# Kernel optimization log

Hardware: AMD Instinct MI355X
Metric: run time of the kernel (lower is better)

## Reference

```python
import jax, jax.numpy as jnp
import numpy as np

LN_EPS = 1e-5


def _layer_norm(x, scale, bias):
    mu = jnp.mean(x, axis=-1, keepdims=True)
    var = jnp.mean(jnp.square(x - mu), axis=-1, keepdims=True)
    return (x - mu) * jax.lax.rsqrt(var + LN_EPS) * scale + bias


def setup_inputs() -> dict:
    key = jax.random.key(0)
    B, N, C_Z, C_H = 1, 512, 128, 128
    ks = jax.random.split(key, 8)
    s = 1.0 / np.sqrt(C_Z)
    inp = {
        "z": jax.random.normal(ks[0], (B, N, N, C_Z), dtype=jnp.float32),
        "mask": jnp.ones((B, N, N), dtype=jnp.float32),
        # gated / plain projections from c_z -> c_hidden
        "w_a_p": jax.random.normal(ks[1], (C_Z, C_H), dtype=jnp.float32) * s,
        "b_a_p": jnp.zeros((C_H,), dtype=jnp.float32),
        "w_a_g": jnp.zeros((C_Z, C_H), dtype=jnp.float32),  # gating init: zeros, bias ones
        "b_a_g": jnp.ones((C_H,), dtype=jnp.float32),
        "w_b_p": jax.random.normal(ks[2], (C_Z, C_H), dtype=jnp.float32) * s,
        "b_b_p": jnp.zeros((C_H,), dtype=jnp.float32),
        "w_b_g": jnp.zeros((C_Z, C_H), dtype=jnp.float32),
        "b_b_g": jnp.ones((C_H,), dtype=jnp.float32),
        # output gate c_z -> c_z (gating init)
        "w_g": jnp.zeros((C_Z, C_Z), dtype=jnp.float32),
        "b_g": jnp.ones((C_Z,), dtype=jnp.float32),
        # final projection c_hidden -> c_z ('final' init: zeros; use small randn for a nontrivial test)
        "w_z": jax.random.normal(ks[3], (C_H, C_Z), dtype=jnp.float32) * (1.0 / np.sqrt(C_H)),
        "b_z": jnp.zeros((C_Z,), dtype=jnp.float32),
        "ln_in_scale": jnp.ones((C_Z,), dtype=jnp.float32),
        "ln_in_bias": jnp.zeros((C_Z,), dtype=jnp.float32),
        "ln_out_scale": jnp.ones((C_H,), dtype=jnp.float32),
        "ln_out_bias": jnp.zeros((C_H,), dtype=jnp.float32),
    }
    return inp


def reference(z, mask, w_a_p, b_a_p, w_a_g, b_a_g, w_b_p, b_b_p, w_b_g, b_b_g,
              w_g, b_g, w_z, b_z, ln_in_scale, ln_in_bias, ln_out_scale, ln_out_bias):
    # tmu_type == 'outgoing'
    z = _layer_norm(z, ln_in_scale, ln_in_bias)          # [B,N,N,Cz]
    m = mask[..., None]                                   # [B,N,N,1]
    a = jax.nn.sigmoid(z @ w_a_g + b_a_g) * m * (z @ w_a_p + b_a_p)  # [B,N,N,Ch]
    b = jax.nn.sigmoid(z @ w_b_g + b_b_g) * m * (z @ w_b_p + b_b_p)  # [B,N,N,Ch]
    # outgoing: p[b,i,j,c] = sum_k a[b,i,k,c] * b[b,j,k,c]
    x = jnp.einsum("bikc,bjkc->bijc", a, b)              # [B,N,N,Ch]
    x = _layer_norm(x, ln_out_scale, ln_out_bias)
    x = x @ w_z + b_z                                    # [B,N,N,Cz]
    g = jax.nn.sigmoid(z @ w_g + b_g)                    # [B,N,N,Cz]
    return x * g
```

## Files before the change

kernel.cpp:

```cpp
#include <hip/hip_runtime.h>

typedef __attribute__((ext_vector_type(8))) short short8;
typedef __attribute__((ext_vector_type(4))) short short4v;
typedef __attribute__((ext_vector_type(4))) float float4v;

#define NDIM 512
#define NN (NDIM*NDIM)
#define CD 128

__device__ __forceinline__ unsigned short f2b(float f) {
  union { float f; unsigned u; } v; v.f = f;
  unsigned r = v.u + 0x7FFFu + ((v.u >> 16) & 1u);
  return (unsigned short)(r >> 16);
}
__device__ __forceinline__ float b2f(unsigned short h) {
  union { unsigned u; float f; } v; v.u = ((unsigned)h) << 16; return v.f;
}
__device__ __forceinline__ float sigmoidf_(float x) { return 1.f / (1.f + __expf(-x)); }
__device__ __forceinline__ unsigned pk2(float a, float b) {
  unsigned r;
  asm("v_cvt_pk_bf16_f32 %0, %1, %2" : "=v"(r) : "v"(a), "v"(b));
  return r;
}
__device__ __forceinline__ float4v mfma16(short8 a, short8 b, float4v c) {
  return __builtin_amdgcn_mfma_f32_16x16x32_bf16(a, b, c, 0, 0, 0);
}
__device__ __forceinline__ void gl_lds16(const short* g, short* l) {
  __builtin_amdgcn_global_load_lds(
      (const __attribute__((address_space(1))) unsigned int*)g,
      (__attribute__((address_space(3))) unsigned int*)l, 16, 0, 0);
}

__device__ __forceinline__ short8 fragr(const short* buf, int row, int j) {
  return *(const short8*)(buf + row * 128 + ((j ^ (row & 15)) << 3));
}
__device__ __forceinline__ void stg_w(short* buf, int row, int ku, unsigned v) {
  *(unsigned*)&buf[row * 128 + ((((ku >> 2) ^ (row & 15)) << 3) + ((ku & 3) << 1))] = v;
}

__global__ __launch_bounds__(256) void kPrepW(
    const float* __restrict__ w0, const float* __restrict__ w1,
    const float* __restrict__ w2, const float* __restrict__ w3,
    const float* __restrict__ w4, short* __restrict__ wt)
{
  const int wi = blockIdx.y;
  const float* W = wi==0 ? w0 : wi==1 ? w1 : wi==2 ? w2 : wi==3 ? w3 : w4;
  const int e = blockIdx.x * 256 + threadIdx.x;
  const int k = e >> 7, n = e & 127;
  wt[wi * 16384 + n * 128 + k] = (short)f2b(W[k * CD + n]);
}

__global__ __launch_bounds__(1024, 4) void kProj(
    const float* __restrict__ z, const float* __restrict__ mask,
    const short* __restrict__ wT,
    const float* __restrict__ b_a_p, const float* __restrict__ b_a_g,
    const float* __restrict__ b_b_p, const float* __restrict__ b_b_g,
    const float* __restrict__ b_g,
    const float* __restrict__ ln_s, const float* __restrict__ ln_b,
    short* __restrict__ a_t, short* __restrict__ b_t, short* __restrict__ g_out)
{
  __shared__ short zln[128 * 128];
  __shared__ short sS[128 * 128];
  __shared__ short wA[128 * 128];
  __shared__ short wB[128 * 128];
  const int t = threadIdx.x;
  const int r0 = blockIdx.x * 128;
  const int w = t >> 6, l = t & 63, lr = l & 15, lg = l >> 4;
  const int wr = (w >> 1) * 16;
  const int hc = (w & 1) * 64;

#define STAGE2(BUF, SLOT) do { _Pragma("unroll") for (int i_=0;i_<2;++i_) {  \
    int U_ = i_*1024 + t; int row_ = U_ >> 4, u_ = U_ & 15;                  \
    gl_lds16(wT + (SLOT)*16384 + row_*128 + ((u_^(row_&15))<<3), (BUF)+U_*8); } } while(0)

  STAGE2(wA, 1);
  STAGE2(wB, 0);

  {
    const int row = t >> 3, q = t & 7;
    const float* zp = z + (size_t)(r0 + row) * CD + q * 16;
    float x[16];
#pragma unroll
    for (int i = 0; i < 4; ++i) {
      float4v v = *(const float4v*)(zp + i * 4);
#pragma unroll
      for (int e = 0; e < 4; ++e) x[i*4+e] = v[e];
    }
    float s = 0.f;
#pragma unroll
    for (int i = 0; i < 16; ++i) s += x[i];
    s += __shfl_xor(s, 1, 64);
    s += __shfl_xor(s, 2, 64);
    s += __shfl_xor(s, 4, 64);
    const float mu = s * (1.f/128.f);
    float vs = 0.f;
#pragma unroll
    for (int i = 0; i < 16; ++i) { float d = x[i]-mu; vs += d*d; }
    vs += __shfl_xor(vs, 1, 64);
    vs += __shfl_xor(vs, 2, 64);
    vs += __shfl_xor(vs, 4, 64);
    const float rstd = rsqrtf(vs * (1.f/128.f) + 1e-5f);
#pragma unroll
    for (int i = 0; i < 16; i += 2) {
      int c = q*16 + i;
      float y0 = (x[i]  -mu)*rstd*ln_s[c]   + ln_b[c];
      float y1 = (x[i+1]-mu)*rstd*ln_s[c+1] + ln_b[c+1];
      int addr = row*128 + (((c>>3) ^ (row & 15)) << 3) + (c & 7);
      *(unsigned*)(&zln[addr]) = pk2(y0, y1);
    }
  }

  float bga[4], bpa[4], bgb[4], bpb[4];
#pragma unroll
  for (int cf = 0; cf < 4; ++cf) {
    int ci = hc + cf*16 + lr;
    bga[cf] = b_a_g[ci]; bpa[cf] = b_a_p[ci];
    bgb[cf] = b_b_g[ci]; bpb[cf] = b_b_p[ci];
  }
  float mrow[4];
#pragma unroll
  for (int jj = 0; jj < 4; ++jj) mrow[jj] = mask[r0 + wr + lg*4 + jj];

  __syncthreads();

  short8 af[4];
#pragma unroll
  for (int ks = 0; ks < 4; ++ks)
    af[ks] = fragr(zln, wr + lr, ks*4 + lg);

  float4v accG[4], accB[4];
  float sg[4][4];

#define ZERO4(A) do { _Pragma("unroll") for (int c_=0;c_<4;++c_) A[c_] = (float4v){0.f,0.f,0.f,0.f}; } while(0)

#define WP(ACC, BUF) do { ZERO4(ACC);                                      \
  _Pragma("unroll") for (int ks_=0; ks_<4; ++ks_)                          \
    _Pragma("unroll") for (int cf_=0; cf_<4; ++cf_) {                      \
      short8 wf_ = fragr(BUF, hc + cf_*16 + lr, ks_*4 + lg);               \
      ACC[cf_] = mfma16(af[ks_], wf_, ACC[cf_]);                           \
    } } while(0)

#define SIG4(BG) do { _Pragma("unroll") for (int cf_=0;cf_<4;++cf_)        \
    _Pragma("unroll") for (int j_=0;j_<4;++j_)                             \
      sg[cf_][j_] = sigmoidf_(accG[cf_][j_] + BG[cf_]) * mrow[j_]; } while(0)

#define PKAB(BP) do { _Pragma("unroll") for (int cf_=0;cf_<4;++cf_) {      \
    float v0_ = sg[cf_][0]*(accB[cf_][0]+BP[cf_]);                         \
    float v1_ = sg[cf_][1]*(accB[cf_][1]+BP[cf_]);                         \
    float v2_ = sg[cf_][2]*(accB[cf_][2]+BP[cf_]);                         \
    float v3_ = sg[cf_][3]*(accB[cf_][3]+BP[cf_]);                         \
    int ch_ = hc + cf_*16 + lr, ku_ = (wr >> 1) + lg*2;                    \
    stg_w(sS, ch_, ku_,   pk2(v0_, v1_));                                  \
    stg_w(sS, ch_, ku_+1, pk2(v2_, v3_)); } } while(0)

#define STORE64A(DST) do { int ch_ = t >> 3;                               \
  _Pragma("unroll") for (int i_=0;i_<2;++i_) {                             \
    int cL_ = (t & 7)*2 + i_;                                              \
    *(short8*)(DST + (size_t)ch_*NN + r0 + cL_*8) = fragr(sS, ch_, cL_);   \
  } } while(0)

  WP(accG, wA);
  WP(accB, wB);
  SIG4(bga);
  PKAB(bpa);
  __syncthreads();

  STAGE2(wA, 3);
  STAGE2(wB, 2);
  STORE64A(a_t);
  __syncthreads();

  WP(accG, wA);
  WP(accB, wB);
  SIG4(bgb);
  PKAB(bpb);
  __syncthreads();

  STAGE2(wA, 4);
  STORE64A(b_t);
  __syncthreads();

  {
    float4v accG2[4];
    ZERO4(accG2);
#pragma unroll
    for (int ks = 0; ks < 4; ++ks)
#pragma unroll
      for (int cf = 0; cf < 4; ++cf) {
        short8 wf = fragr(wA, hc + cf*16 + lr, ks*4 + lg);
        accG2[cf] = mfma16(wf, af[ks], accG2[cf]);
      }
#pragma unroll
    for (int cf = 0; cf < 4; ++cf) {
      float4v bgv = *(const float4v*)(b_g + hc + cf*16 + lg*4);
      float v0 = sigmoidf_(accG2[cf][0] + bgv[0]);
      float v1 = sigmoidf_(accG2[cf][1] + bgv[1]);
      float v2 = sigmoidf_(accG2[cf][2] + bgv[2]);
      float v3 = sigmoidf_(accG2[cf][3] + bgv[3]);
      int row = wr + lr, ku = (hc >> 1) + cf*8 + lg*2;
      stg_w(sS, row, ku,   pk2(v0, v1));
      stg_w(sS, row, ku+1, pk2(v2, v3));
    }
  }
  __syncthreads();

  {
    int row = t >> 3;
#pragma unroll
    for (int i = 0; i < 2; ++i) {
      int cL = (t & 7)*2 + i;
      *(short8*)(g_out + (size_t)(r0 + row)*CD + cL*8) = fragr(sS, row, cL);
    }
  }
}

__global__ __launch_bounds__(256, 2) void kEinsum(const short* __restrict__ a_t,
                                                  const short* __restrict__ b_t,
                                                  short* __restrict__ x_t)
{
  __shared__ short As[2][128 * 64];
  __shared__ short Bs[2][128 * 64];
  const int t = threadIdx.x;
  const int d = blockIdx.x;
  const int c = (d & 7) * 16 + (d >> 7);
  const int tile = (d >> 3) & 15;
  const int i0 = (tile >> 2) * 128;
  const int j0 = (tile & 3) * 128;
  const size_t abase = (size_t)c * NN;
  const int w = t >> 6, l = t & 63, lr = l & 15, lg = l >> 4;
  const int wr = w >> 1, wc = w & 1;

  const short* gA[4]; const short* gB[4]; int ldsU[4];
#pragma unroll
  for (int q = 0; q < 4; ++q) {
    int U = q * 256 + t;
    int row = U >> 3, u = U & 7;
    int swz = ((u ^ (row & 7)) << 3);
    gA[q] = a_t + abase + (size_t)(i0 + row) * NDIM + swz;
    gB[q] = b_t + abase + (size_t)(j0 + row) * NDIM + swz;
    ldsU[q] = U * 8;
  }

#define STAGE_E(buf, k0) do { _Pragma("unroll") for (int q_=0;q_<4;++q_) { \
    gl_lds16(gA[q_] + (k0), &As[buf][ldsU[q_]]);                           \
    gl_lds16(gB[q_] + (k0), &Bs[buf][ldsU[q_]]); } } while(0)

  float4v acc[4][4];
#pragma unroll
  for (int m = 0; m < 4; ++m)
#pragma unroll
    for (int n = 0; n < 4; ++n) acc[m][n] = (float4v){0.f,0.f,0.f,0.f};

  STAGE_E(0, 0);
  STAGE_E(1, 64);
#pragma unroll
  for (int it = 0; it < 8; ++it) {
    if (it < 7) asm volatile("s_waitcnt vmcnt(8)" ::: "memory");
    else        asm volatile("s_waitcnt vmcnt(0)" ::: "memory");
    __builtin_amdgcn_sched_barrier(0);
    __builtin_amdgcn_s_barrier();
    const short* Ab = &As[it & 1][0];
    const short* Bb = &Bs[it & 1][0];
    short8 afr[4][2], bfr[4][2];
#pragma unroll
    for (int m = 0; m < 4; ++m)
#pragma unroll
      for (int ks = 0; ks < 2; ++ks) {
        int row = wr*64 + m*16 + lr, j = ks*4 + lg;
        afr[m][ks] = *(const short8*)(Ab + row*64 + ((j ^ (row & 7)) << 3));
      }
#pragma unroll
    for (int n = 0; n < 4; ++n)
#pragma unroll
      for (int ks = 0; ks < 2; ++ks) {
        int row = wc*64 + n*16 + lr, j = ks*4 + lg;
        bfr[n][ks] = *(const short8*)(Bb + row*64 + ((j ^ (row & 7)) << 3));
      }
    __builtin_amdgcn_s_setprio(1);
#pragma unroll
    for (int ks = 0; ks < 2; ++ks)
#pragma unroll
      for (int m = 0; m < 4; ++m)
#pragma unroll
        for (int n = 0; n < 4; ++n)
          acc[m][n] = mfma16(bfr[n][ks], afr[m][ks], acc[m][n]);
    __builtin_amdgcn_s_setprio(0);
    __builtin_amdgcn_s_barrier();
    __builtin_amdgcn_sched_barrier(0);
    if (it < 6) STAGE_E(it & 1, (it + 2) * 64);
  }
  short* Xs = &As[0][0];
#pragma unroll
  for (int m = 0; m < 4; ++m)
#pragma unroll
    for (int n = 0; n < 4; ++n) {
      int il = wr*64 + m*16 + lr;
      int ku = wc*32 + n*8 + lg*2;
      stg_w(Xs, il, ku,   pk2(acc[m][n][0], acc[m][n][1]));
      stg_w(Xs, il, ku+1, pk2(acc[m][n][2], acc[m][n][3]));
    }
  __syncthreads();
#pragma unroll
  for (int i = 0; i < 8; ++i) {
    int il = t >> 1, cL = (t & 1)*8 + i;
    *(short8*)(x_t + abase + (size_t)(i0 + il)*NDIM + j0 + cL*8) = fragr(Xs, il, cL);
  }
}

__global__ __launch_bounds__(256, 2) void kOut(
    const short* __restrict__ x_t, const short* __restrict__ g_in,
    const float* __restrict__ w_z, const float* __restrict__ b_z,
    const float* __restrict__ ln_s, const float* __restrict__ ln_b,
    float* __restrict__ out)
{
  __shared__ short xs[128 * 72];
  __shared__ short xln[64 * 128];
  __shared__ short sW[128 * 128];
  const int t = threadIdx.x;
  const int r0 = blockIdx.x * 64;
  const int w = t >> 6, l = t & 63, lr = l & 15, lg = l >> 4;

#pragma unroll
  for (int i = 0; i < 8; ++i) {
    int flat = i * 256 + t;
    int kp = flat >> 5, k = kp * 2, n4 = (flat & 31) * 4;
    float4v va = *(const float4v*)(w_z + (size_t)k * CD + n4);
    float4v vb = *(const float4v*)(w_z + (size_t)(k + 1) * CD + n4);
#pragma unroll
    for (int j = 0; j < 4; ++j) {
      int row = n4 + j;
      int addr = row * 128 + (((k >> 3) ^ (row & 15)) << 3) + (k & 7);
      *(unsigned*)(&sW[addr]) = pk2(va[j], vb[j]);
    }
  }
#pragma unroll
  for (int it = 0; it < 4; ++it) {
    int v = it * 256 + t; int cc = v >> 3; int u = v & 7;
    int up = u ^ ((cc >> 3) & 7);
    *(short8*)&xs[cc * 72 + up * 8] = *(const short8*)(x_t + (size_t)cc * NN + r0 + u * 8);
  }
  __syncthreads();
  {
    const int r = t >> 2, q = t & 3;
    float x[32];
#pragma unroll
    for (int i = 0; i < 32; ++i) {
      int c = q * 32 + i;
      x[i] = b2f((unsigned short)xs[c * 72 + (((r >> 3) ^ ((c >> 3) & 7)) << 3) + (r & 7)]);
    }
    float s = 0.f;
#pragma unroll
    for (int i = 0; i < 32; ++i) s += x[i];
    s += __shfl_xor(s, 1, 64);
    s += __shfl_xor(s, 2, 64);
    const float mu = s * (1.f/128.f);
    float vs = 0.f;
#pragma unroll
    for (int i = 0; i < 32; ++i) { float d = x[i]-mu; vs += d*d; }
    vs += __shfl_xor(vs, 1, 64);
    vs += __shfl_xor(vs, 2, 64);
    const float rstd = rsqrtf(vs * (1.f/128.f) + 1e-5f);
#pragma unroll
    for (int i = 0; i < 32; ++i) {
      int c = q*32 + i;
      float y = (x[i]-mu)*rstd*ln_s[c] + ln_b[c];
      xln[r*128 + (((c>>3) ^ (r & 15)) << 3) + (c & 7)] = (short)f2b(y);
    }
  }
  __syncthreads();
  short8 af[4];
#pragma unroll
  for (int ks = 0; ks < 4; ++ks)
    af[ks] = fragr(xln, w*16 + lr, ks*4 + lg);

  float4v acc[8];
#pragma unroll
  for (int cf = 0; cf < 8; ++cf) acc[cf] = (float4v){0.f,0.f,0.f,0.f};
#pragma unroll
  for (int ks = 0; ks < 4; ++ks)
#pragma unroll
    for (int cf = 0; cf < 8; ++cf) {
      short8 wf = fragr(sW, cf*16 + lr, ks*4 + lg);
      acc[cf] = mfma16(wf, af[ks], acc[cf]);
    }
  __syncthreads();
  float* fWs = (float*)sW;
  const int orow = r0 + w*16 + lr;
  const int rl = w*16 + lr;
#pragma unroll
  for (int cf = 0; cf < 8; ++cf) {
    float4v bzv = *(const float4v*)(b_z + cf*16 + lg*4);
    short4v gv = *(const short4v*)(g_in + (size_t)orow * CD + cf*16 + lg*4);
    float4v o;
#pragma unroll
    for (int j = 0; j < 4; ++j)
      o[j] = (acc[cf][j] + bzv[j]) * b2f((unsigned short)gv[j]);
    *(float4v*)&fWs[rl*128 + (((cf*4+lg) ^ (rl & 15)) << 2)] = o;
  }
  __syncthreads();
#pragma unroll
  for (int i = 0; i < 8; ++i) {
    int row = t >> 2, cL = (t & 3)*8 + i;
    *(float4v*)(out + (size_t)(r0 + row)*CD + cL*4) =
        *(const float4v*)&fWs[row*128 + ((cL ^ (row & 15)) << 2)];
  }
}

extern "C" void kernel_launch(void* const* d_in, const int* in_sizes, int n_in,
                              void* d_out, int out_size, void* d_ws, size_t ws_size,
                              hipStream_t stream) {
  (void)in_sizes; (void)n_in; (void)out_size; (void)ws_size;
  const float* z     = (const float*)d_in[0];
  const float* mask  = (const float*)d_in[1];
  const float* w_a_p = (const float*)d_in[2];
  const float* b_a_p = (const float*)d_in[3];
  const float* w_a_g = (const float*)d_in[4];
  const float* b_a_g = (const float*)d_in[5];
  const float* w_b_p = (const float*)d_in[6];
  const float* b_b_p = (const float*)d_in[7];
  const float* w_b_g = (const float*)d_in[8];
  const float* b_b_g = (const float*)d_in[9];
  const float* w_g   = (const float*)d_in[10];
  const float* b_g   = (const float*)d_in[11];
  const float* w_z   = (const float*)d_in[12];
  const float* b_z   = (const float*)d_in[13];
  const float* ln_i_s = (const float*)d_in[14];
  const float* ln_i_b = (const float*)d_in[15];
  const float* ln_o_s = (const float*)d_in[16];
  const float* ln_o_b = (const float*)d_in[17];

  short* a_t = (short*)d_ws;
  short* b_t = a_t + (size_t)CD*NN;
  short* g_s = b_t + (size_t)CD*NN;
  short* x_t = g_s + (size_t)CD*NN;
  short* wT  = x_t;

  hipLaunchKernelGGL(kPrepW, dim3(64, 5), dim3(256), 0, stream,
                     w_a_p, w_a_g, w_b_p, w_b_g, w_g, wT);
  hipLaunchKernelGGL(kProj, dim3(NN/128), dim3(1024), 0, stream,
                     z, mask, wT, b_a_p, b_a_g, b_b_p, b_b_g, b_g,
                     ln_i_s, ln_i_b, a_t, b_t, g_s);
  hipLaunchKernelGGL(kEinsum, dim3(2048), dim3(256), 0, stream, a_t, b_t, x_t);
  hipLaunchKernelGGL(kOut, dim3(NN/64), dim3(256), 0, stream,
                     x_t, g_s, w_z, b_z, ln_o_s, ln_o_b, (float*)d_out);
}
```

Measured before the change: 346.7 us.

## Restructure output kernel to 128-row tiles with 1024 threads and async loads

The output-projection kernel now processes 128 rows per block with 1024 threads, so each block stages the w_z matrix once for twice as many rows. The x tile is loaded into LDS with gl_lds16, and the gate values are prefetched into registers early and then staged in LDS. The MFMA operand order is swapped so the epilogue writes out directly from registers instead of going through an LDS transpose. The per-element scalar stores may coalesce worse, and the larger LDS footprint per block (about 96KB) limits occupancy.

```diff
diff --git a/kernel.cpp b/kernel.cpp
--- a/kernel.cpp
+++ b/kernel.cpp
@@ -307,22 +307,35 @@
   }
 }
 
-__global__ __launch_bounds__(256, 2) void kOut(
+__global__ __launch_bounds__(1024, 4) void kOut(
     const short* __restrict__ x_t, const short* __restrict__ g_in,
     const float* __restrict__ w_z, const float* __restrict__ b_z,
     const float* __restrict__ ln_s, const float* __restrict__ ln_b,
     float* __restrict__ out)
 {
-  __shared__ short xs[128 * 72];
-  __shared__ short xln[64 * 128];
+  __shared__ short xs[128 * 128];
+  __shared__ short xln[128 * 128];
   __shared__ short sW[128 * 128];
   const int t = threadIdx.x;
-  const int r0 = blockIdx.x * 64;
+  const int r0 = blockIdx.x * 128;
   const int w = t >> 6, l = t & 63, lr = l & 15, lg = l >> 4;
-
-#pragma unroll
-  for (int i = 0; i < 8; ++i) {
-    int flat = i * 256 + t;
+  const int rowb = (w >> 1) * 16;
+  const int hc = (w & 1) * 64;
+
+  short8 gv[2];
+#pragma unroll
+  for (int v = 0; v < 2; ++v) {
+    int V = v*1024 + t; int row = V >> 4, u = V & 15;
+    gv[v] = *(const short8*)(g_in + (size_t)(r0 + row) * CD + u * 8);
+  }
+#pragma unroll
+  for (int v = 0; v < 2; ++v) {
+    int U = v*1024 + t; int cc = U >> 4, u = U & 15;
+    gl_lds16(x_t + (size_t)cc * NN + r0 + ((u ^ ((cc >> 3) & 15)) << 3), xs + U*8);
+  }
+#pragma unroll
+  for (int i = 0; i < 2; ++i) {
+    int flat = i*1024 + t;
     int kp = flat >> 5, k = kp * 2, n4 = (flat & 31) * 4;
     float4v va = *(const float4v*)(w_z + (size_t)k * CD + n4);
     float4v vb = *(const float4v*)(w_z + (size_t)(k + 1) * CD + n4);
@@ -333,76 +346,72 @@
       *(unsigned*)(&sW[addr]) = pk2(va[j], vb[j]);
     }
   }
-#pragma unroll
-  for (int it = 0; it < 4; ++it) {
-    int v = it * 256 + t; int cc = v >> 3; int u = v & 7;
-    int up = u ^ ((cc >> 3) & 7);
-    *(short8*)&xs[cc * 72 + up * 8] = *(const short8*)(x_t + (size_t)cc * NN + r0 + u * 8);
-  }
   __syncthreads();
   {
-    const int r = t >> 2, q = t & 3;
-    float x[32];
-#pragma unroll
-    for (int i = 0; i < 32; ++i) {
-      int c = q * 32 + i;
-      x[i] = b2f((unsigned short)xs[c * 72 + (((r >> 3) ^ ((c >> 3) & 7)) << 3) + (r & 7)]);
+    const int r = t >> 3, q = t & 7;
+    float x[16];
+#pragma unroll
+    for (int i = 0; i < 16; ++i) {
+      int c = q*16 + i;
+      x[i] = b2f((unsigned short)xs[c*128 + (((r >> 3) ^ ((c >> 3) & 15)) << 3) + (r & 7)]);
     }
     float s = 0.f;
 #pragma unroll
-    for (int i = 0; i < 32; ++i) s += x[i];
+    for (int i = 0; i < 16; ++i) s += x[i];
     s += __shfl_xor(s, 1, 64);
     s += __shfl_xor(s, 2, 64);
+    s += __shfl_xor(s, 4, 64);
     const float mu = s * (1.f/128.f);
     float vs = 0.f;
 #pragma unroll
-    for (int i = 0; i < 32; ++i) { float d = x[i]-mu; vs += d*d; }
+    for (int i = 0; i < 16; ++i) { float d = x[i]-mu; vs += d*d; }
     vs += __shfl_xor(vs, 1, 64);
     vs += __shfl_xor(vs, 2, 64);
+    vs += __shfl_xor(vs, 4, 64);
     const float rstd = rsqrtf(vs * (1.f/128.f) + 1e-5f);
 #pragma unroll
-    for (int i = 0; i < 32; ++i) {
-      int c = q*32 + i;
-      float y = (x[i]-mu)*rstd*ln_s[c] + ln_b[c];
-      xln[r*128 + (((c>>3) ^ (r & 15)) << 3) + (c & 7)] = (short)f2b(y);
-    }
-  }
-  __syncthreads();
+    for (int i = 0; i < 16; i += 2) {
+      int c = q*16 + i;
+      float y0 = (x[i]  -mu)*rstd*ln_s[c]   + ln_b[c];
+      float y1 = (x[i+1]-mu)*rstd*ln_s[c+1] + ln_b[c+1];
+      int addr = r*128 + (((c>>3) ^ (r & 15)) << 3) + (c & 7);
+      *(unsigned*)(&xln[addr]) = pk2(y0, y1);
+    }
+  }
+  __syncthreads();
+  short* sG = xs;
+#pragma unroll
+  for (int v = 0; v < 2; ++v) {
+    int V = v*1024 + t; int row = V >> 4, u = V & 15;
+    *(short8*)(sG + row*128 + ((u ^ (row & 15)) << 3)) = gv[v];
+  }
   short8 af[4];
 #pragma unroll
   for (int ks = 0; ks < 4; ++ks)
-    af[ks] = fragr(xln, w*16 + lr, ks*4 + lg);
-
-  float4v acc[8];
-#pragma unroll
-  for (int cf = 0; cf < 8; ++cf) acc[cf] = (float4v){0.f,0.f,0.f,0.f};
+    af[ks] = fragr(xln, rowb + lr, ks*4 + lg);
+  float4v acc[4];
+#pragma unroll
+  for (int cf = 0; cf < 4; ++cf) acc[cf] = (float4v){0.f,0.f,0.f,0.f};
 #pragma unroll
   for (int ks = 0; ks < 4; ++ks)
 #pragma unroll
-    for (int cf = 0; cf < 8; ++cf) {
-      short8 wf = fragr(sW, cf*16 + lr, ks*4 + lg);
-      acc[cf] = mfma16(wf, af[ks], acc[cf]);
-    }
-  __syncthreads();
-  float* fWs = (float*)sW;
-  const int orow = r0 + w*16 + lr;
-  const int rl = w*16 + lr;
-#pragma unroll
-  for (int cf = 0; cf < 8; ++cf) {
-    float4v bzv = *(const float4v*)(b_z + cf*16 + lg*4);
-    short4v gv = *(const short4v*)(g_in + (size_t)orow * CD + cf*16 + lg*4);
-    float4v o;
-#pragma unroll
-    for (int j = 0; j < 4; ++j)
-      o[j] = (acc[cf][j] + bzv[j]) * b2f((unsigned short)gv[j]);
-    *(float4v*)&fWs[rl*128 + (((cf*4+lg) ^ (rl & 15)) << 2)] = o;
-  }
-  __syncthreads();
-#pragma unroll
-  for (int i = 0; i < 8; ++i) {
-    int row = t >> 2, cL = (t & 3)*8 + i;
-    *(float4v*)(out + (size_t)(r0 + row)*CD + cL*4) =
-        *(const float4v*)&fWs[row*128 + ((cL ^ (row & 15)) << 2)];
+    for (int cf = 0; cf < 4; ++cf) {
+      short8 wf = fragr(sW, hc + cf*16 + lr, ks*4 + lg);
+      acc[cf] = mfma16(af[ks], wf, acc[cf]);
+    }
+  float bz[4];
+#pragma unroll
+  for (int cf = 0; cf < 4; ++cf) bz[cf] = b_z[hc + cf*16 + lr];
+  __syncthreads();
+#pragma unroll
+  for (int cf = 0; cf < 4; ++cf) {
+    int ch = hc + cf*16 + lr;
+#pragma unroll
+    for (int jj = 0; jj < 4; ++jj) {
+      int row = rowb + lg*4 + jj;
+      float gvv = b2f((unsigned short)sG[row*128 + (((ch>>3) ^ (row & 15)) << 3) + (ch & 7)]);
+      out[(size_t)(r0 + row) * CD + ch] = (acc[cf][jj] + bz[cf]) * gvv;
+    }
   }
 }
 
@@ -441,6 +450,6 @@
                      z, mask, wT, b_a_p, b_a_g, b_b_p, b_b_g, b_g,
                      ln_i_s, ln_i_b, a_t, b_t, g_s);
   hipLaunchKernelGGL(kEinsum, dim3(2048), dim3(256), 0, stream, a_t, b_t, x_t);
-  hipLaunchKernelGGL(kOut, dim3(NN/64), dim3(256), 0, stream,
+  hipLaunchKernelGGL(kOut, dim3(NN/128), dim3(1024), 0, stream,
                      x_t, g_s, w_z, b_z, ln_o_s, ln_o_b, (float*)d_out);
 }
```

Result: faster. 312.3 us (-9.9%).
